# Kernel optimization log

Measured on AMD Instinct MI355X. Metric: run time of the kernel, lower is better.

The kernel has to match this reference:

```python
import jax, jax.numpy as jnp
import numpy as np

B, L, D, H = 2, 4096, 512, 8
HD = D // H
SCALE = 1.0 / (D / H) ** 0.5


def setup_inputs() -> dict:
    key = jax.random.key(0)
    ks = jax.random.split(key, 12)
    s = 0.02
    inp = {
        "q": jax.random.normal(ks[0], (B, L, D), jnp.float32),
        "k": jax.random.normal(ks[1], (B, L, D), jnp.float32),
        "v": jax.random.normal(ks[2], (B, L, D), jnp.float32),
        # causal mask, True = keep (masked_fill where mask == False)
        "mask": jnp.tril(jnp.ones((L, L), bool))[None, None, :, :],
        "Wq": jax.random.normal(ks[3], (D, D), jnp.float32) * s,
        "bq": jnp.zeros((D,), jnp.float32),
        "Wk": jax.random.normal(ks[4], (D, D), jnp.float32) * s,
        "bk": jnp.zeros((D,), jnp.float32),
        "Wv": jax.random.normal(ks[5], (D, D), jnp.float32) * s,
        "bv": jnp.zeros((D,), jnp.float32),
        "Wo": jax.random.normal(ks[6], (D, D), jnp.float32) * s,
        "bo": jnp.zeros((D,), jnp.float32),
    }
    return inp


def _split_heads(x):
    # [B, L, D] -> [B, H, L, HD]
    b, l, d = x.shape
    return x.reshape(b, l, H, HD).transpose(0, 2, 1, 3)


def reference(q, k, v, mask, Wq, bq, Wk, bk, Wv, bv, Wo, bo):
    # Dropout is inference-mode (identity), matching module.eval().
    qh = _split_heads(q @ Wq.T + bq)          # [B,H,L,HD]
    kh = _split_heads(k @ Wk.T + bk)          # [B,H,L,HD]
    vh = _split_heads(v @ Wv.T + bv)          # [B,H,L,HD]
    scores = jnp.einsum("bhqd,bhkd->bhqk", qh, kh) * SCALE
    scores = jnp.where(mask, scores, -jnp.inf)
    attn = jax.nn.softmax(scores, axis=-1)
    out = jnp.einsum("bhqk,bhkd->bhqd", attn, vh)  # [B,H,L,HD]
    out = out.transpose(0, 2, 1, 3).reshape(q.shape[0], q.shape[1], D)
    return out @ Wo.T + bo
```

## Files before the change

kernel.cpp:

```cpp
#include <hip/hip_runtime.h>

typedef __bf16 bf16;
typedef __bf16 bf16x4 __attribute__((ext_vector_type(4)));
typedef __bf16 bf16x8 __attribute__((ext_vector_type(8)));
typedef float  f32x4  __attribute__((ext_vector_type(4)));
typedef float  f32x16 __attribute__((ext_vector_type(16)));
typedef unsigned int u32x2 __attribute__((ext_vector_type(2)));
typedef unsigned int u32x4 __attribute__((ext_vector_type(4)));

#define NB   2
#define NL   4096
#define ND   512
#define NH   8
#define NHD  64

static __device__ __forceinline__ void g2l16(const bf16* g, bf16* l) {
    __builtin_amdgcn_global_load_lds(
        (const __attribute__((address_space(1))) unsigned int*)g,
        (__attribute__((address_space(3))) unsigned int*)l, 16, 0, 0);
}

__global__ __launch_bounds__(256) void cvt_all(
    const float* __restrict__ q, const float* __restrict__ k, const float* __restrict__ v,
    const float* __restrict__ Wq, const float* __restrict__ Wk,
    const float* __restrict__ Wv, const float* __restrict__ Wo,
    bf16* __restrict__ qb, bf16* __restrict__ kb, bf16* __restrict__ vb,
    bf16* __restrict__ wqb, bf16* __restrict__ wkb,
    bf16* __restrict__ wvb, bf16* __restrict__ wob)
{
    const int z = blockIdx.z;
    const float* src; bf16* dst; int n4;
    switch (z) {
        case 0: src = q;  dst = qb;  n4 = NB * NL * ND / 4; break;
        case 1: src = k;  dst = kb;  n4 = NB * NL * ND / 4; break;
        case 2: src = v;  dst = vb;  n4 = NB * NL * ND / 4; break;
        case 3: src = Wq; dst = wqb; n4 = ND * ND / 4; break;
        case 4: src = Wk; dst = wkb; n4 = ND * ND / 4; break;
        case 5: src = Wv; dst = wvb; n4 = ND * ND / 4; break;
        default: src = Wo; dst = wob; n4 = ND * ND / 4; break;
    }
    for (int i = blockIdx.x * 256 + threadIdx.x; i < n4; i += gridDim.x * 256) {
        const f32x4 a = *(const f32x4*)(src + (size_t)i * 4);
        bf16x4 o;
        #pragma unroll
        for (int j = 0; j < 4; ++j) o[j] = (bf16)a[j];
        *(bf16x4*)(dst + (size_t)i * 4) = o;
    }
}

__global__ __launch_bounds__(256, 1) void proj_qkv(
    const bf16* __restrict__ qb, const bf16* __restrict__ kb, const bf16* __restrict__ vb,
    const bf16* __restrict__ wq, const bf16* __restrict__ wk, const bf16* __restrict__ wv,
    const float* __restrict__ biasq, const float* __restrict__ biask, const float* __restrict__ biasv,
    bf16* __restrict__ qh, bf16* __restrict__ kh, bf16* __restrict__ vt)
{
    const int z = blockIdx.z;
    const bf16* X     = (z == 0) ? qb : (z == 1) ? kb : vb;
    const bf16* W     = (z == 0) ? wq : (z == 1) ? wk : wv;
    const float* bias = (z == 0) ? biasq : (z == 1) ? biask : biasv;

    const int m0 = blockIdx.y * 128;
    const int n0 = blockIdx.x * 128;

    __shared__ bf16 smem[65536];

    const int t    = threadIdx.x;
    const int lane = t & 63;
    const int wm   = (t >> 7) & 1;
    const int wn   = (t >> 6) & 1;
    const int quad = lane >> 4;
    const int l16  = lane & 15;

    auto stage = [&](int k0, int buf) {
        #pragma unroll
        for (int p = 0; p < 8; ++p) {
            const int id = p * 256 + t;
            const int r = id >> 4, s = id & 15;
            const int c = (s ^ (r & 7)) * 8;
            g2l16(X + (size_t)(m0 + r) * ND + k0 + c, smem + buf * 16384 + id * 8);
            g2l16(W + (size_t)(n0 + r) * ND + k0 + c, smem + 32768 + buf * 16384 + id * 8);
        }
    };

    f32x4 acc[4][4] = {};
    stage(0, 0);

    for (int it = 0; it < 4; ++it) {
        __syncthreads();
        if (it + 1 < 4) stage((it + 1) * 128, (it + 1) & 1);

        const bf16* as = smem + (it & 1) * 16384;
        const bf16* bs = smem + 32768 + (it & 1) * 16384;
        #pragma unroll
        for (int kk = 0; kk < 4; ++kk) {
            bf16x8 aF[4], bF[4];
            #pragma unroll
            for (int i = 0; i < 4; ++i) {
                const int ra = wm * 64 + i * 16 + l16;
                const int rb = wn * 64 + i * 16 + l16;
                aF[i] = *(const bf16x8*)(as + ra * 128 + (((kk * 4 + quad) ^ (ra & 7)) * 8));
                bF[i] = *(const bf16x8*)(bs + rb * 128 + (((kk * 4 + quad) ^ (rb & 7)) * 8));
            }
            #pragma unroll
            for (int mt = 0; mt < 4; ++mt)
                #pragma unroll
                for (int nt = 0; nt < 4; ++nt)
                    acc[mt][nt] = __builtin_amdgcn_mfma_f32_16x16x32_bf16(
                        aF[mt], bF[nt], acc[mt][nt], 0, 0, 0);
        }
    }

    __syncthreads();
    const float oscale = (z == 0) ? 0.125f : (z == 1) ? 1.4426950408889634f : 1.0f;
    const int b = m0 >> 12;
    const int l0 = m0 & 4095;
    bf16* Cs = smem;

    if (z == 2) {
        #pragma unroll
        for (int nt = 0; nt < 4; ++nt) {
            const int col = wn * 64 + nt * 16 + l16;
            const float bb = bias[n0 + col];
            #pragma unroll
            for (int mt = 0; mt < 4; ++mt) {
                const int rowm = wm * 64 + mt * 16 + quad * 4;
                #pragma unroll
                for (int rb = 0; rb < 4; ++rb)
                    Cs[col * 136 + rowm + rb] = (bf16)(acc[mt][nt][rb] + bb);
            }
        }
        __syncthreads();
        #pragma unroll
        for (int p = 0; p < 8; ++p) {
            const int id = p * 256 + t;
            const int c = id >> 4, kc = id & 15;
            const int gcol = n0 + c;
            const int h = gcol >> 6, hd = gcol & 63;
            const bf16x8 v8 = *(const bf16x8*)(Cs + c * 136 + kc * 8);
            *(bf16x8*)(vt + ((size_t)(b * NH + h) * NHD + hd) * NL + l0 + kc * 8) = v8;
        }
    } else {
        #pragma unroll
        for (int nt = 0; nt < 4; ++nt) {
            const int col = wn * 64 + nt * 16 + l16;
            const float bb = bias[n0 + col];
            #pragma unroll
            for (int mt = 0; mt < 4; ++mt) {
                const int rowm = wm * 64 + mt * 16 + quad * 4;
                #pragma unroll
                for (int rb = 0; rb < 4; ++rb)
                    Cs[(rowm + rb) * 136 + col] = (bf16)((acc[mt][nt][rb] + bb) * oscale);
            }
        }
        __syncthreads();
        bf16* dst = (z == 0) ? qh : kh;
        const int h0 = n0 >> 6;
        #pragma unroll
        for (int p = 0; p < 8; ++p) {
            const int id = p * 256 + t;
            const int r = id >> 4, j = (id >> 3) & 1, kc = id & 7;
            const bf16x8 v8 = *(const bf16x8*)(Cs + r * 136 + j * 64 + kc * 8);
            *(bf16x8*)(dst + ((size_t)(b * NH + h0 + j) * NL + l0 + r) * NHD + kc * 8) = v8;
        }
    }
}

__global__ __launch_bounds__(512, 2) void attn(
    const bf16* __restrict__ qh, const bf16* __restrict__ kh,
    const bf16* __restrict__ vt, bf16* __restrict__ ao)
{
    const int bh  = blockIdx.x;
    const int b   = bh >> 3, h = bh & 7;
    const int qtA = blockIdx.y;
    const int qtB = 31 - qtA;
    const int nAp = qtA + 1;

    __shared__ bf16 smem[65536];

    const int t    = threadIdx.x;
    const int wave = t >> 6;
    const int g    = wave >> 2;
    const int w4   = wave & 3;
    const int lane = t & 63;
    const int l32  = lane & 31;
    const int half = lane >> 5;
    const int sb   = g * 32768;
    const int tg   = t & 255;

    const bf16* Qg = qh + (size_t)bh * NL * NHD;
    const bf16* Kg = kh + (size_t)bh * NL * NHD;
    const bf16* Vg = vt + (size_t)bh * NHD * NL;

    #pragma unroll
    for (int p = 0; p < 4; ++p) {
        const int id = p * 512 + t;
        const int tile = id >> 10, r = (id >> 3) & 127, s = id & 7;
        const int q0 = (tile ? qtB : qtA) * 128;
        g2l16(Qg + (size_t)(q0 + r) * NHD + s * 8, smem + id * 8);
    }
    __syncthreads();

    bf16x8 qf[4];
    {
        const int qoff = (g == 0) ? 8192 : 0;
        #pragma unroll
        for (int c = 0; c < 4; ++c)
            qf[c] = *(const bf16x8*)(smem + qoff + (w4 * 32 + l32) * 64 + c * 16 + half * 8);
    }
    __syncthreads();

    auto stage_kv = [&](int k0, int buf) {
        bf16* kd = smem + sb + buf * 16384;
        bf16* vd = kd + 8192;
        #pragma unroll
        for (int p = 0; p < 4; ++p) {
            const int id = p * 256 + tg;
            const int r = id >> 3, s = id & 7;
            g2l16(Kg + (size_t)(k0 + r) * NHD + ((s ^ (r & 7)) * 8), kd + id * 8);
            const int ks2 = id >> 9, idh = id & 511;
            const int r2 = idh >> 3, s2 = idh & 7;
            g2l16(Vg + (size_t)r2 * NL + k0 + ks2 * 64 + ((s2 ^ (r2 & 7)) * 8),
                  vd + id * 8);
        }
    };

    stage_kv(((g == 0) ? (15 - qtA) : 0) * 128, 0);

    f32x16 o_acc[2] = {};
    float l_lane = 0.f;

    for (int jj = 0; jj < 17; ++jj) {
        __syncthreads();

        if (jj + 1 < 17) {
            const int jn = jj + 1;
            if (g == 0)          stage_kv((15 - qtA + jn) * 128, jn & 1);
            else if (jn < 16)    stage_kv(((jn < nAp) ? jn : jn - nAp) * 128, jn & 1);
        }

        if (g == 1 && jj == nAp) {
            const float lt = l_lane + __shfl_xor(l_lane, 32, 64);
            const float rcp = 1.0f / fmaxf(lt, 1e-20f);
            const int row = qtA * 128 + w4 * 32 + l32;
            #pragma unroll
            for (int mt2 = 0; mt2 < 2; ++mt2)
                #pragma unroll
                for (int rr = 0; rr < 4; ++rr) {
                    const int hd = mt2 * 32 + rr * 8 + half * 4;
                    bf16x4 val;
                    #pragma unroll
                    for (int rb = 0; rb < 4; ++rb)
                        val[rb] = (bf16)(o_acc[mt2][rr * 4 + rb] * rcp);
                    *(bf16x4*)(ao + ((size_t)b * NL + row) * ND + h * NHD + hd) = val;
                }
            o_acc[0] = (f32x16)(0.f); o_acc[1] = (f32x16)(0.f);
            l_lane = 0.f;
            const bf16* Qt = Qg + (size_t)(qtB * 128 + w4 * 32 + l32) * NHD;
            #pragma unroll
            for (int c = 0; c < 4; ++c)
                qf[c] = *(const bf16x8*)(Qt + c * 16 + half * 8);
        }

        const bool act = (g == 0) || (jj < 16);
        if (act) {
            const bool onA   = (g == 1) && (jj < nAp);
            const int tile   = (g == 0) ? (15 - qtA + jj) : (onA ? jj : jj - nAp);
            const int qt_cur = onA ? qtA : qtB;
            const bf16* kb_ = smem + sb + (jj & 1) * 16384;
            const bf16* vb_ = kb_ + 8192;
            const int qrow_l = w4 * 32 + l32;

            #pragma unroll
            for (int ksub = 0; ksub < 2; ++ksub) {
                const bf16* ks_ = kb_ + ksub * 4096;
                const bf16* vs_ = vb_ + ksub * 4096;
                const int j64 = tile * 2 + ksub;

                f32x16 sacc[2] = {};
                #pragma unroll
                for (int c = 0; c < 4; ++c) {
                    #pragma unroll
                    for (int mt = 0; mt < 2; ++mt) {
                        const int row   = mt * 32 + l32;
                        const int chunk = 2 * c + half;
                        const bf16x8 kf = *(const bf16x8*)(ks_ + row * 64 + ((chunk ^ (row & 7)) * 8));
                        sacc[mt] = __builtin_amdgcn_mfma_f32_32x32x16_bf16(
                            kf, qf[c], sacc[mt], 0, 0, 0);
                    }
                }

                const bool diag = (j64 >= 2 * qt_cur);
                const int  dq   = j64 * 64 - qt_cur * 128;
                #pragma unroll
                for (int mt = 0; mt < 2; ++mt) {
                    #pragma unroll
                    for (int r = 0; r < 16; ++r) {
                        const int kv = mt * 32 + (r & 3) + 8 * (r >> 2) + 4 * half;
                        float e;
                        if (diag && (dq + kv > qrow_l)) e = 0.f;
                        else e = __builtin_amdgcn_exp2f(sacc[mt][r]);
                        l_lane += e;
                        sacc[mt][r] = e;
                    }
                }

                #pragma unroll
                for (int c = 0; c < 4; ++c) {
                    const int mt = c >> 1;
                    const int b0 = (c & 1) * 8;
                    unsigned w0, w1, w2, w3;
                    asm("v_cvt_pk_bf16_f32 %0, %1, %2" : "=v"(w0)
                        : "v"(sacc[mt][b0 + 0]), "v"(sacc[mt][b0 + 1]));
                    asm("v_cvt_pk_bf16_f32 %0, %1, %2" : "=v"(w1)
                        : "v"(sacc[mt][b0 + 2]), "v"(sacc[mt][b0 + 3]));
                    asm("v_cvt_pk_bf16_f32 %0, %1, %2" : "=v"(w2)
                        : "v"(sacc[mt][b0 + 4]), "v"(sacc[mt][b0 + 5]));
                    asm("v_cvt_pk_bf16_f32 %0, %1, %2" : "=v"(w3)
                        : "v"(sacc[mt][b0 + 6]), "v"(sacc[mt][b0 + 7]));
                    const u32x2 s02 = __builtin_amdgcn_permlane32_swap(w0, w2, false, false);
                    const u32x2 s13 = __builtin_amdgcn_permlane32_swap(w1, w3, false, false);
                    u32x4 pw_ = { s02.x, s13.x, s02.y, s13.y };
                    bf16x8 pf;
                    __builtin_memcpy(&pf, &pw_, 16);
                    #pragma unroll
                    for (int mt2 = 0; mt2 < 2; ++mt2) {
                        const int row = mt2 * 32 + l32;
                        const int u8  = 2 * c + half;
                        const bf16x8 vf = *(const bf16x8*)(vs_ + row * 64 + ((u8 ^ (row & 7)) * 8));
                        o_acc[mt2] = __builtin_amdgcn_mfma_f32_32x32x16_bf16(
                            vf, pf, o_acc[mt2], 0, 0, 0);
                    }
                }
            }
        }
    }

    __syncthreads();
    float* comb = (float*)smem;
    if (g == 1) {
        const int base = w4 * (64 * 36) + lane * 36;
        #pragma unroll
        for (int mt2 = 0; mt2 < 2; ++mt2)
            #pragma unroll
            for (int i = 0; i < 16; ++i)
                comb[base + mt2 * 16 + i] = o_acc[mt2][i];
        const float lt = l_lane + __shfl_xor(l_lane, 32, 64);
        if (half == 0) comb[9216 + w4 * 32 + l32] = lt;
    }
    __syncthreads();
    if (g == 0) {
        const int base = w4 * (64 * 36) + lane * 36;
        const float lt = l_lane + __shfl_xor(l_lane, 32, 64)
                       + comb[9216 + w4 * 32 + l32];
        const float rcp = 1.0f / fmaxf(lt, 1e-20f);
        const int row = qtB * 128 + w4 * 32 + l32;
        #pragma unroll
        for (int mt2 = 0; mt2 < 2; ++mt2)
            #pragma unroll
            for (int rr = 0; rr < 4; ++rr) {
                const int hd = mt2 * 32 + rr * 8 + half * 4;
                bf16x4 val;
                #pragma unroll
                for (int rb = 0; rb < 4; ++rb)
                    val[rb] = (bf16)((o_acc[mt2][rr * 4 + rb] +
                                      comb[base + mt2 * 16 + rr * 4 + rb]) * rcp);
                *(bf16x4*)(ao + ((size_t)b * NL + row) * ND + h * NHD + hd) = val;
            }
    }
}

__global__ __launch_bounds__(256, 1) void out_proj(
    const bf16* __restrict__ ao, const bf16* __restrict__ wo,
    const float* __restrict__ bo, float* __restrict__ out)
{
    const int m0 = blockIdx.y * 128;
    const int n0 = blockIdx.x * 128;

    __shared__ bf16 smem[65536];

    const int t    = threadIdx.x;
    const int lane = t & 63;
    const int wm   = (t >> 7) & 1;
    const int wn   = (t >> 6) & 1;
    const int quad = lane >> 4;
    const int l16  = lane & 15;

    auto stage = [&](int k0, int buf) {
        #pragma unroll
        for (int p = 0; p < 8; ++p) {
            const int id = p * 256 + t;
            const int r = id >> 4, s = id & 15;
            const int c = (s ^ (r & 7)) * 8;
            g2l16(ao + (size_t)(m0 + r) * ND + k0 + c, smem + buf * 16384 + id * 8);
            g2l16(wo + (size_t)(n0 + r) * ND + k0 + c, smem + 32768 + buf * 16384 + id * 8);
        }
    };

    f32x4 acc[4][4] = {};
    stage(0, 0);

    for (int it = 0; it < 4; ++it) {
        __syncthreads();
        if (it + 1 < 4) stage((it + 1) * 128, (it + 1) & 1);

        const bf16* as = smem + (it & 1) * 16384;
        const bf16* bs = smem + 32768 + (it & 1) * 16384;
        #pragma unroll
        for (int kk = 0; kk < 4; ++kk) {
            bf16x8 aF[4], bF[4];
            #pragma unroll
            for (int i = 0; i < 4; ++i) {
                const int ra = wm * 64 + i * 16 + l16;
                const int rb = wn * 64 + i * 16 + l16;
                aF[i] = *(const bf16x8*)(as + ra * 128 + (((kk * 4 + quad) ^ (ra & 7)) * 8));
                bF[i] = *(const bf16x8*)(bs + rb * 128 + (((kk * 4 + quad) ^ (rb & 7)) * 8));
            }
            #pragma unroll
            for (int mt = 0; mt < 4; ++mt)
                #pragma unroll
                for (int nt = 0; nt < 4; ++nt)
                    acc[mt][nt] = __builtin_amdgcn_mfma_f32_16x16x32_bf16(
                        aF[mt], bF[nt], acc[mt][nt], 0, 0, 0);
        }
    }

    __syncthreads();
    float* Cs = (float*)smem;
    #pragma unroll
    for (int nt = 0; nt < 4; ++nt) {
        const int col = wn * 64 + nt * 16 + l16;
        const float bb = bo[n0 + col];
        #pragma unroll
        for (int mt = 0; mt < 4; ++mt) {
            const int rowm = wm * 64 + mt * 16 + quad * 4;
            #pragma unroll
            for (int rb = 0; rb < 4; ++rb)
                Cs[(rowm + rb) * 132 + col] = acc[mt][nt][rb] + bb;
        }
    }
    __syncthreads();
    #pragma unroll
    for (int p = 0; p < 16; ++p) {
        const int id = p * 256 + t;
        const int r = id >> 5, kc = id & 31;
        const f32x4 v4 = *(const f32x4*)(Cs + r * 132 + kc * 4);
        *(f32x4*)(out + (size_t)(m0 + r) * ND + n0 + kc * 4) = v4;
    }
}

extern "C" void kernel_launch(void* const* d_in, const int* in_sizes, int n_in,
                              void* d_out, int out_size, void* d_ws, size_t ws_size,
                              hipStream_t stream) {
    (void)in_sizes; (void)n_in; (void)out_size; (void)ws_size;

    const float* q  = (const float*)d_in[0];
    const float* k  = (const float*)d_in[1];
    const float* v  = (const float*)d_in[2];
    const float* Wq = (const float*)d_in[4];
    const float* bq = (const float*)d_in[5];
    const float* Wk = (const float*)d_in[6];
    const float* bk = (const float*)d_in[7];
    const float* Wv = (const float*)d_in[8];
    const float* bv = (const float*)d_in[9];
    const float* Wo = (const float*)d_in[10];
    const float* bo = (const float*)d_in[11];

    const size_t XSZ = (size_t)NB * NL * ND;
    const size_t WSZ = (size_t)ND * ND;
    bf16* p = (bf16*)d_ws;
    bf16* qb  = p; p += XSZ;
    bf16* kb  = p; p += XSZ;
    bf16* vb  = p; p += XSZ;
    bf16* wqb = p; p += WSZ;
    bf16* wkb = p; p += WSZ;
    bf16* wvb = p; p += WSZ;
    bf16* wob = p; p += WSZ;
    bf16* qh  = p; p += XSZ;
    bf16* kh  = p; p += XSZ;
    bf16* vt  = p; p += XSZ;
    bf16* ao  = p; p += XSZ;

    cvt_all<<<dim3(512, 1, 7), 256, 0, stream>>>(
        q, k, v, Wq, Wk, Wv, Wo, qb, kb, vb, wqb, wkb, wvb, wob);

    dim3 g1(ND / 128, (NB * NL) / 128, 3);
    proj_qkv<<<g1, 256, 0, stream>>>(qb, kb, vb, wqb, wkb, wvb, bq, bk, bv, qh, kh, vt);

    dim3 g2(16, 16, 1);
    attn<<<g2, 512, 0, stream>>>(qh, kh, vt, ao);

    dim3 g3(ND / 128, (NB * NL) / 128, 1);
    out_proj<<<g3, 256, 0, stream>>>(ao, wob, bo, (float*)d_out);
}
```

Measured before the change: 242.8 us.

## Fuse fp32-to-bf16 conversion into projection GEMM loads, drop separate convert kernel

Removes the standalone cvt_all kernel. The QKV and output projection GEMMs now read fp32 inputs and weights through registers, convert them to bf16, and write them into swizzled LDS, using a register-staged double buffer with a K tile of 64. This saves one kernel launch and a full write and reread of bf16 copies of q, k and v. The cost is that the asynchronous global-to-LDS loads become register round trips with more register pressure, and the weights are converted again by every block. The shared-memory footprint per block is halved so two blocks can fit per CU.

```diff
diff --git a/kernel.cpp b/kernel.cpp
--- a/kernel.cpp
+++ b/kernel.cpp
@@ -20,49 +20,21 @@
         (__attribute__((address_space(3))) unsigned int*)l, 16, 0, 0);
 }
 
-__global__ __launch_bounds__(256) void cvt_all(
+__global__ __launch_bounds__(256, 2) void proj_qkv(
     const float* __restrict__ q, const float* __restrict__ k, const float* __restrict__ v,
-    const float* __restrict__ Wq, const float* __restrict__ Wk,
-    const float* __restrict__ Wv, const float* __restrict__ Wo,
-    bf16* __restrict__ qb, bf16* __restrict__ kb, bf16* __restrict__ vb,
-    bf16* __restrict__ wqb, bf16* __restrict__ wkb,
-    bf16* __restrict__ wvb, bf16* __restrict__ wob)
-{
-    const int z = blockIdx.z;
-    const float* src; bf16* dst; int n4;
-    switch (z) {
-        case 0: src = q;  dst = qb;  n4 = NB * NL * ND / 4; break;
-        case 1: src = k;  dst = kb;  n4 = NB * NL * ND / 4; break;
-        case 2: src = v;  dst = vb;  n4 = NB * NL * ND / 4; break;
-        case 3: src = Wq; dst = wqb; n4 = ND * ND / 4; break;
-        case 4: src = Wk; dst = wkb; n4 = ND * ND / 4; break;
-        case 5: src = Wv; dst = wvb; n4 = ND * ND / 4; break;
-        default: src = Wo; dst = wob; n4 = ND * ND / 4; break;
-    }
-    for (int i = blockIdx.x * 256 + threadIdx.x; i < n4; i += gridDim.x * 256) {
-        const f32x4 a = *(const f32x4*)(src + (size_t)i * 4);
-        bf16x4 o;
-        #pragma unroll
-        for (int j = 0; j < 4; ++j) o[j] = (bf16)a[j];
-        *(bf16x4*)(dst + (size_t)i * 4) = o;
-    }
-}
-
-__global__ __launch_bounds__(256, 1) void proj_qkv(
-    const bf16* __restrict__ qb, const bf16* __restrict__ kb, const bf16* __restrict__ vb,
-    const bf16* __restrict__ wq, const bf16* __restrict__ wk, const bf16* __restrict__ wv,
+    const float* __restrict__ Wq, const float* __restrict__ Wk, const float* __restrict__ Wv,
     const float* __restrict__ biasq, const float* __restrict__ biask, const float* __restrict__ biasv,
     bf16* __restrict__ qh, bf16* __restrict__ kh, bf16* __restrict__ vt)
 {
     const int z = blockIdx.z;
-    const bf16* X     = (z == 0) ? qb : (z == 1) ? kb : vb;
-    const bf16* W     = (z == 0) ? wq : (z == 1) ? wk : wv;
+    const float* X    = (z == 0) ? q : (z == 1) ? k : v;
+    const float* W    = (z == 0) ? Wq : (z == 1) ? Wk : Wv;
     const float* bias = (z == 0) ? biasq : (z == 1) ? biask : biasv;
 
     const int m0 = blockIdx.y * 128;
     const int n0 = blockIdx.x * 128;
 
-    __shared__ bf16 smem[65536];
+    __shared__ bf16 smem[32768];
 
     const int t    = threadIdx.x;
     const int lane = t & 63;
@@ -71,35 +43,51 @@
     const int quad = lane >> 4;
     const int l16  = lane & 15;
 
-    auto stage = [&](int k0, int buf) {
-        #pragma unroll
-        for (int p = 0; p < 8; ++p) {
-            const int id = p * 256 + t;
-            const int r = id >> 4, s = id & 15;
-            const int c = (s ^ (r & 7)) * 8;
-            g2l16(X + (size_t)(m0 + r) * ND + k0 + c, smem + buf * 16384 + id * 8);
-            g2l16(W + (size_t)(n0 + r) * ND + k0 + c, smem + 32768 + buf * 16384 + id * 8);
+    f32x4 ta[8], tb[8];
+    auto issue = [&](int k0) {
+        #pragma unroll
+        for (int p = 0; p < 8; ++p) {
+            const int c4 = p * 256 + t;
+            const int r = c4 >> 4, cs = c4 & 15;
+            ta[p] = *(const f32x4*)(X + (size_t)(m0 + r) * ND + k0 + cs * 4);
+            tb[p] = *(const f32x4*)(W + (size_t)(n0 + r) * ND + k0 + cs * 4);
         }
     };
+    auto commit = [&](int buf) {
+        bf16* Ad = smem + buf * 8192;
+        bf16* Bd = smem + 16384 + buf * 8192;
+        #pragma unroll
+        for (int p = 0; p < 8; ++p) {
+            const int c4 = p * 256 + t;
+            const int r = c4 >> 4, cs = c4 & 15;
+            const int addr = r * 64 + (((cs >> 1) ^ (r & 7)) * 8) + (cs & 1) * 4;
+            bf16x4 a4, b4;
+            #pragma unroll
+            for (int j = 0; j < 4; ++j) { a4[j] = (bf16)ta[p][j]; b4[j] = (bf16)tb[p][j]; }
+            *(bf16x4*)(Ad + addr) = a4;
+            *(bf16x4*)(Bd + addr) = b4;
+        }
+    };
 
     f32x4 acc[4][4] = {};
-    stage(0, 0);
-
-    for (int it = 0; it < 4; ++it) {
+    issue(0);
+
+    for (int it = 0; it < 8; ++it) {
+        commit(it & 1);
         __syncthreads();
-        if (it + 1 < 4) stage((it + 1) * 128, (it + 1) & 1);
-
-        const bf16* as = smem + (it & 1) * 16384;
-        const bf16* bs = smem + 32768 + (it & 1) * 16384;
-        #pragma unroll
-        for (int kk = 0; kk < 4; ++kk) {
+        if (it + 1 < 8) issue((it + 1) * 64);
+
+        const bf16* as = smem + (it & 1) * 8192;
+        const bf16* bs = smem + 16384 + (it & 1) * 8192;
+        #pragma unroll
+        for (int kk = 0; kk < 2; ++kk) {
             bf16x8 aF[4], bF[4];
             #pragma unroll
             for (int i = 0; i < 4; ++i) {
                 const int ra = wm * 64 + i * 16 + l16;
                 const int rb = wn * 64 + i * 16 + l16;
-                aF[i] = *(const bf16x8*)(as + ra * 128 + (((kk * 4 + quad) ^ (ra & 7)) * 8));
-                bF[i] = *(const bf16x8*)(bs + rb * 128 + (((kk * 4 + quad) ^ (rb & 7)) * 8));
+                aF[i] = *(const bf16x8*)(as + ra * 64 + (((kk * 4 + quad) ^ (ra & 7)) * 8));
+                bF[i] = *(const bf16x8*)(bs + rb * 64 + (((kk * 4 + quad) ^ (rb & 7)) * 8));
             }
             #pragma unroll
             for (int mt = 0; mt < 4; ++mt)
@@ -369,14 +357,14 @@
     }
 }
 
-__global__ __launch_bounds__(256, 1) void out_proj(
-    const bf16* __restrict__ ao, const bf16* __restrict__ wo,
+__global__ __launch_bounds__(256, 2) void out_proj(
+    const bf16* __restrict__ ao, const float* __restrict__ wo,
     const float* __restrict__ bo, float* __restrict__ out)
 {
     const int m0 = blockIdx.y * 128;
     const int n0 = blockIdx.x * 128;
 
-    __shared__ bf16 smem[65536];
+    __shared__ bf16 smem[34816];
 
     const int t    = threadIdx.x;
     const int lane = t & 63;
@@ -385,35 +373,62 @@
     const int quad = lane >> 4;
     const int l16  = lane & 15;
 
-    auto stage = [&](int k0, int buf) {
-        #pragma unroll
-        for (int p = 0; p < 8; ++p) {
-            const int id = p * 256 + t;
-            const int r = id >> 4, s = id & 15;
-            const int c = (s ^ (r & 7)) * 8;
-            g2l16(ao + (size_t)(m0 + r) * ND + k0 + c, smem + buf * 16384 + id * 8);
-            g2l16(wo + (size_t)(n0 + r) * ND + k0 + c, smem + 32768 + buf * 16384 + id * 8);
+    bf16x8 va[4];
+    f32x4  tb[8];
+    auto issue = [&](int k0) {
+        #pragma unroll
+        for (int p = 0; p < 4; ++p) {
+            const int c8 = p * 256 + t;
+            const int r = c8 >> 3, s = c8 & 7;
+            va[p] = *(const bf16x8*)(ao + (size_t)(m0 + r) * ND + k0 + s * 8);
+        }
+        #pragma unroll
+        for (int p = 0; p < 8; ++p) {
+            const int c4 = p * 256 + t;
+            const int r = c4 >> 4, cs = c4 & 15;
+            tb[p] = *(const f32x4*)(wo + (size_t)(n0 + r) * ND + k0 + cs * 4);
         }
     };
+    auto commit = [&](int buf) {
+        bf16* Ad = smem + buf * 8192;
+        bf16* Bd = smem + 16384 + buf * 8192;
+        #pragma unroll
+        for (int p = 0; p < 4; ++p) {
+            const int c8 = p * 256 + t;
+            const int r = c8 >> 3, s = c8 & 7;
+            *(bf16x8*)(Ad + r * 64 + ((s ^ (r & 7)) * 8)) = va[p];
+        }
+        #pragma unroll
+        for (int p = 0; p < 8; ++p) {
+            const int c4 = p * 256 + t;
+            const int r = c4 >> 4, cs = c4 & 15;
+            const int addr = r * 64 + (((cs >> 1) ^ (r & 7)) * 8) + (cs & 1) * 4;
+            bf16x4 b4;
+            #pragma unroll
+            for (int j = 0; j < 4; ++j) b4[j] = (bf16)tb[p][j];
+            *(bf16x4*)(Bd + addr) = b4;
+        }
+    };
 
     f32x4 acc[4][4] = {};
-    stage(0, 0);
-
-    for (int it = 0; it < 4; ++it) {
+    issue(0);
+
+    for (int it = 0; it < 8; ++it) {
+        commit(it & 1);
         __syncthreads();
-        if (it + 1 < 4) stage((it + 1) * 128, (it + 1) & 1);
-
-        const bf16* as = smem + (it & 1) * 16384;
-        const bf16* bs = smem + 32768 + (it & 1) * 16384;
-        #pragma unroll
-        for (int kk = 0; kk < 4; ++kk) {
+        if (it + 1 < 8) issue((it + 1) * 64);
+
+        const bf16* as = smem + (it & 1) * 8192;
+        const bf16* bs = smem + 16384 + (it & 1) * 8192;
+        #pragma unroll
+        for (int kk = 0; kk < 2; ++kk) {
             bf16x8 aF[4], bF[4];
             #pragma unroll
             for (int i = 0; i < 4; ++i) {
                 const int ra = wm * 64 + i * 16 + l16;
                 const int rb = wn * 64 + i * 16 + l16;
-                aF[i] = *(const bf16x8*)(as + ra * 128 + (((kk * 4 + quad) ^ (ra & 7)) * 8));
-                bF[i] = *(const bf16x8*)(bs + rb * 128 + (((kk * 4 + quad) ^ (rb & 7)) * 8));
+                aF[i] = *(const bf16x8*)(as + ra * 64 + (((kk * 4 + quad) ^ (ra & 7)) * 8));
+                bF[i] = *(const bf16x8*)(bs + rb * 64 + (((kk * 4 + quad) ^ (rb & 7)) * 8));
             }
             #pragma unroll
             for (int mt = 0; mt < 4; ++mt)
@@ -466,29 +481,18 @@
     const float* bo = (const float*)d_in[11];
 
     const size_t XSZ = (size_t)NB * NL * ND;
-    const size_t WSZ = (size_t)ND * ND;
     bf16* p = (bf16*)d_ws;
-    bf16* qb  = p; p += XSZ;
-    bf16* kb  = p; p += XSZ;
-    bf16* vb  = p; p += XSZ;
-    bf16* wqb = p; p += WSZ;
-    bf16* wkb = p; p += WSZ;
-    bf16* wvb = p; p += WSZ;
-    bf16* wob = p; p += WSZ;
     bf16* qh  = p; p += XSZ;
     bf16* kh  = p; p += XSZ;
     bf16* vt  = p; p += XSZ;
     bf16* ao  = p; p += XSZ;
 
-    cvt_all<<<dim3(512, 1, 7), 256, 0, stream>>>(
-        q, k, v, Wq, Wk, Wv, Wo, qb, kb, vb, wqb, wkb, wvb, wob);
-
     dim3 g1(ND / 128, (NB * NL) / 128, 3);
-    proj_qkv<<<g1, 256, 0, stream>>>(qb, kb, vb, wqb, wkb, wvb, bq, bk, bv, qh, kh, vt);
+    proj_qkv<<<g1, 256, 0, stream>>>(q, k, v, Wq, Wk, Wv, bq, bk, bv, qh, kh, vt);
 
     dim3 g2(16, 16, 1);
     attn<<<g2, 512, 0, stream>>>(qh, kh, vt, ao);
 
     dim3 g3(ND / 128, (NB * NL) / 128, 1);
-    out_proj<<<g3, 256, 0, stream>>>(ao, wob, bo, (float*)d_out);
+    out_proj<<<g3, 256, 0, stream>>>(ao, Wo, bo, (float*)d_out);
 }
```

New measurement: 248.7 us. 2.4% more time.
